# Kernel optimization log

Measured on AMD Instinct MI355X. Metric: run time of the kernel, lower is better.

The kernel has to match this reference:

```python
import jax, jax.numpy as jnp
import numpy as np

MEAN = jnp.array([0.0, 0.0, 0.0, 0.0, 0.0], dtype=jnp.float32)
STD = jnp.array([0.1, 0.1, 0.2, 0.2, 1.0], dtype=jnp.float32)


def setup_inputs() -> dict:
    key = jax.random.key(0)
    k1, k2 = jax.random.split(key)
    B, N = 8, 250000
    boxes = jax.random.normal(k1, (B, N, 5), dtype=jnp.float32)
    deltas = jax.random.normal(k2, (B, N, 5), dtype=jnp.float32)
    return {"boxes": boxes, "deltas": deltas}


def reference(boxes, deltas):
    B, N = boxes.shape[0], boxes.shape[1]
    widths = boxes[:, :, 2] - boxes[:, :, 0]
    heights = boxes[:, :, 3] - boxes[:, :, 1]
    ctr_x = boxes[:, :, 0] + 0.5 * widths
    ctr_y = boxes[:, :, 1] + 0.5 * heights
    alpha = boxes[:, :, 4]

    d = deltas * STD + MEAN  # fused elementwise denorm
    dx, dy, dw, dh, dalpha = d[:, :, 0], d[:, :, 1], d[:, :, 2], d[:, :, 3], d[:, :, 4]

    pred_ctr_x = ctr_x + dx * widths
    pred_ctr_y = ctr_y + dy * heights
    pred_w = jnp.exp(dw) * widths
    pred_h = jnp.exp(dh) * heights
    pred_alpha = jnp.arctan(dalpha) + alpha

    x1 = pred_ctr_x - 0.5 * pred_w
    y1 = pred_ctr_y - 0.5 * pred_h
    x4 = pred_ctr_x + 0.5 * pred_w
    y4 = pred_ctr_y + 0.5 * pred_h
    x2 = x1
    y2 = y4
    x3 = x4
    y3 = y1

    ones = jnp.ones_like(y4)
    # Faithful to original: torch.cat along dim 0 then view(B,N,3,4)
    pred_boxes = jnp.concatenate(
        [x1, x2, x3, x4, y1, y2, y3, y4, ones, ones, ones, ones], axis=0
    ).reshape(B, N, 3, 4)

    z = jnp.zeros_like(pred_ctr_x)
    o = jnp.ones_like(pred_ctr_x)
    # 3x3 homogeneous matrices, built along last axis (matches torch dim=-1 cat)
    T = jnp.stack([o, z, pred_ctr_x, z, o, pred_ctr_y, z, z, o], axis=-1).reshape(B, N, 3, 3)
    Tinv = jnp.stack([o, z, -pred_ctr_x, z, o, -pred_ctr_y, z, z, o], axis=-1).reshape(B, N, 3, 3)
    ca, sa = jnp.cos(pred_alpha), jnp.sin(pred_alpha)
    R = jnp.stack([ca, -sa, z, sa, ca, z, z, z, o], axis=-1).reshape(B, N, 3, 3)

    # [B,N,3,3] @ [B,N,3,4] chain, keep xy rows, transpose corners-last -> xy-last
    bbox_rotated = jnp.matmul(T, jnp.matmul(R, jnp.matmul(Tinv, pred_boxes)))[:, :, :2]
    return jnp.swapaxes(bbox_rotated, 2, 3)  # [B, N, 4, 2]
```

## Files before the change

kernel.cpp:

```cpp
#include <hip/hip_runtime.h>


typedef float    f4v __attribute__((ext_vector_type(4)));
typedef _Float16 h4v __attribute__((ext_vector_type(4)));
typedef _Float16 h8v __attribute__((ext_vector_type(8)));

__global__ __launch_bounds__(256) void bbox_phase1(
    const float* __restrict__ boxes, const float* __restrict__ deltas,
    _Float16* __restrict__ V, _Float16* __restrict__ CTR, int N, int total)
{
    int t = blockIdx.x * blockDim.x + threadIdx.x;
    int i0 = t * 4;
    if (i0 >= total) return;
    int b = i0 / N;
    int c = i0 - b * N;

    bool fast = (i0 + 3 < total) && (c + 3 < N) && ((c & 3) == 0) && ((N & 3) == 0);
    if (fast) {
        const f4v* bp = (const f4v*)(boxes  + (size_t)i0 * 5);
        const f4v* dp = (const f4v*)(deltas + (size_t)i0 * 5);
        float bv[20], dv[20];
        *(f4v*)&bv[0]  = bp[0]; *(f4v*)&bv[4]  = bp[1]; *(f4v*)&bv[8]  = bp[2];
        *(f4v*)&bv[12] = bp[3]; *(f4v*)&bv[16] = bp[4];
        *(f4v*)&dv[0]  = dp[0]; *(f4v*)&dv[4]  = dp[1]; *(f4v*)&dv[8]  = dp[2];
        *(f4v*)&dv[12] = dp[3]; *(f4v*)&dv[16] = dp[4];

        float X1[4], X4[4], Y1[4], Y4[4], PX[4], PY[4], CA[4], SA[4];
#pragma unroll
        for (int j = 0; j < 4; ++j) {
            float b0 = bv[j*5+0], b1 = bv[j*5+1], b2 = bv[j*5+2],
                  b3 = bv[j*5+3], b4 = bv[j*5+4];
            float d0 = dv[j*5+0], d1 = dv[j*5+1], d2 = dv[j*5+2],
                  d3 = dv[j*5+3], d4 = dv[j*5+4];
            float w  = b2 - b0, h = b3 - b1;
            float pcx = b0 + 0.5f * w + (d0 * 0.1f) * w;
            float pcy = b1 + 0.5f * h + (d1 * 0.1f) * h;
            float pw  = __expf(d2 * 0.2f) * w;
            float ph  = __expf(d3 * 0.2f) * h;
            X1[j] = pcx - 0.5f * pw;  X4[j] = pcx + 0.5f * pw;
            Y1[j] = pcy - 0.5f * ph;  Y4[j] = pcy + 0.5f * ph;
            float pal = atanf(d4) + b4;
            PX[j] = pcx; PY[j] = pcy;
            SA[j] = __sinf(pal); CA[j] = __cosf(pal);
        }
        size_t rs = (size_t)N;
        *(h4v*)(V + (size_t)(0*8 + b) * rs + c) =
            (h4v){(_Float16)X1[0],(_Float16)X1[1],(_Float16)X1[2],(_Float16)X1[3]};
        *(h4v*)(V + (size_t)(1*8 + b) * rs + c) =
            (h4v){(_Float16)X4[0],(_Float16)X4[1],(_Float16)X4[2],(_Float16)X4[3]};
        *(h4v*)(V + (size_t)(2*8 + b) * rs + c) =
            (h4v){(_Float16)Y1[0],(_Float16)Y1[1],(_Float16)Y1[2],(_Float16)Y1[3]};
        *(h4v*)(V + (size_t)(3*8 + b) * rs + c) =
            (h4v){(_Float16)Y4[0],(_Float16)Y4[1],(_Float16)Y4[2],(_Float16)Y4[3]};
        h8v ctrA = {(_Float16)PX[0],(_Float16)PY[0],(_Float16)CA[0],(_Float16)SA[0],
                    (_Float16)PX[1],(_Float16)PY[1],(_Float16)CA[1],(_Float16)SA[1]};
        h8v ctrB = {(_Float16)PX[2],(_Float16)PY[2],(_Float16)CA[2],(_Float16)SA[2],
                    (_Float16)PX[3],(_Float16)PY[3],(_Float16)CA[3],(_Float16)SA[3]};
        *(h8v*)(CTR + (size_t)i0 * 4)     = ctrA;
        *(h8v*)(CTR + (size_t)i0 * 4 + 8) = ctrB;
    } else {
#pragma unroll 1
        for (int j = 0; j < 4; ++j) {
            int i = i0 + j;
            if (i >= total) break;
            int bb = i / N, cc = i - bb * N;
            const float* bx = boxes  + (size_t)i * 5;
            const float* dl = deltas + (size_t)i * 5;
            float b0=bx[0],b1=bx[1],b2=bx[2],b3=bx[3],b4=bx[4];
            float d0=dl[0],d1=dl[1],d2=dl[2],d3=dl[3],d4=dl[4];
            float w = b2-b0, h = b3-b1;
            float pcx = b0 + 0.5f*w + (d0*0.1f)*w;
            float pcy = b1 + 0.5f*h + (d1*0.1f)*h;
            float pw = __expf(d2*0.2f)*w, ph = __expf(d3*0.2f)*h;
            size_t rs = (size_t)N;
            V[(size_t)(0*8+bb)*rs + cc] = (_Float16)(pcx - 0.5f*pw);
            V[(size_t)(1*8+bb)*rs + cc] = (_Float16)(pcx + 0.5f*pw);
            V[(size_t)(2*8+bb)*rs + cc] = (_Float16)(pcy - 0.5f*ph);
            V[(size_t)(3*8+bb)*rs + cc] = (_Float16)(pcy + 0.5f*ph);
            float pal = atanf(d4) + b4;
            CTR[(size_t)i*4 + 0] = (_Float16)pcx;
            CTR[(size_t)i*4 + 1] = (_Float16)pcy;
            CTR[(size_t)i*4 + 2] = (_Float16)__cosf(pal);
            CTR[(size_t)i*4 + 3] = (_Float16)__sinf(pal);
        }
    }
}

__global__ __launch_bounds__(256) void bbox_phase2(
    const _Float16* __restrict__ V, const _Float16* __restrict__ CTR,
    float* __restrict__ out, int N, int total)
{
    int t = blockIdx.x * blockDim.x + threadIdx.x;
    int i0 = t * 2;
    if (i0 >= total) return;

    int f = i0 * 12;
    int r = f / N;
    int c = f - r * N;
    bool pair = (i0 + 1 < total);

    float P[24];
    bool fast = pair && (c + 23 < N) && ((c & 7) == 0);
    if (fast) {
        if (r < 64) {
            int k = r >> 3, bb = r & 7;
            int v = (k < 4) ? (k >> 1) : (2 + (k & 1));
            const h8v* wp = (const h8v*)(V + (size_t)(v*8 + bb) * N + c);
            h8v a = wp[0], d = wp[1], e = wp[2];
#pragma unroll
            for (int j = 0; j < 8; ++j) {
                P[j]      = (float)a[j];
                P[8 + j]  = (float)d[j];
                P[16 + j] = (float)e[j];
            }
        } else {
#pragma unroll
            for (int j = 0; j < 24; ++j) P[j] = 1.0f;
        }
    } else {
#pragma unroll 1
        for (int j = 0; j < 24; ++j) {
            if (!pair && j >= 12) { P[j] = 1.0f; continue; }
            int ff = f + j;
            int rt = ff / N;
            int ct = ff - rt * N;
            if (rt >= 64) { P[j] = 1.0f; }
            else {
                int k = rt >> 3, bb = rt & 7;
                int v = (k < 4) ? (k >> 1) : (2 + (k & 1));
                P[j] = (float)V[(size_t)(v*8 + bb) * N + ct];
            }
        }
    }

    float pcx[2], pcy[2], cav[2], sav[2];
    if (pair) {
        h8v cc = *(const h8v*)(CTR + (size_t)i0 * 4);
        pcx[0]=(float)cc[0]; pcy[0]=(float)cc[1]; cav[0]=(float)cc[2]; sav[0]=(float)cc[3];
        pcx[1]=(float)cc[4]; pcy[1]=(float)cc[5]; cav[1]=(float)cc[6]; sav[1]=(float)cc[7];
    } else {
        pcx[0]=(float)CTR[(size_t)i0*4+0]; pcy[0]=(float)CTR[(size_t)i0*4+1];
        cav[0]=(float)CTR[(size_t)i0*4+2]; sav[0]=(float)CTR[(size_t)i0*4+3];
        pcx[1]=0.f; pcy[1]=0.f; cav[1]=1.f; sav[1]=0.f;
    }

#pragma unroll
    for (int q = 0; q < 2; ++q) {
        if (q && !pair) break;
        float r0o[4], r1o[4];
#pragma unroll
        for (int j = 0; j < 4; ++j) {
            float p0 = P[q*12 + j], p1 = P[q*12 + 4 + j], p2 = P[q*12 + 8 + j];
            float u0 = p0 - pcx[q] * p2;
            float u1 = p1 - pcy[q] * p2;
            float v0 = cav[q] * u0 - sav[q] * u1;
            float v1 = sav[q] * u0 + cav[q] * u1;
            r0o[j] = v0 + pcx[q] * p2;
            r1o[j] = v1 + pcy[q] * p2;
        }
        f4v* op = (f4v*)(out + (size_t)(i0 + q) * 8);
        op[0] = (f4v){r0o[0], r1o[0], r0o[1], r1o[1]};
        op[1] = (f4v){r0o[2], r1o[2], r0o[3], r1o[3]};
    }
}

__global__ __launch_bounds__(256) void bbox_fused_fallback(
    const float* __restrict__ boxes, const float* __restrict__ deltas,
    float* __restrict__ out, int N, int total)
{
    int idx = blockIdx.x * blockDim.x + threadIdx.x;
    if (idx >= total) return;
    int bp = idx / N;
    int n  = idx - bp * N;
    const float* bx = boxes  + (size_t)idx * 5;
    const float* dl = deltas + (size_t)idx * 5;
    float b0=bx[0],b1=bx[1],b2=bx[2],b3=bx[3],b4=bx[4];
    float d0=dl[0],d1=dl[1],d4=dl[4];
    float w=b2-b0, h=b3-b1;
    float pcx = b0+0.5f*w+(d0*0.1f)*w;
    float pcy = b1+0.5f*h+(d1*0.1f)*h;
    float pal = atanf(d4)+b4;
    float sa = __sinf(pal), ca = __cosf(pal);
    int m0 = n*12, q = m0/N, c0 = m0-q*N, r0 = bp*12+q;
    float P[12];
#pragma unroll
    for (int t = 0; t < 12; ++t) {
        int c = c0+t, r = r0;
        if (c >= N) { c -= N; r += 1; }
        float v;
        if (r >= 64) v = 1.0f;
        else {
            int k = r>>3, b = r&7;
            size_t base = ((size_t)b*N + c)*5;
            int a = (k<4)?0:1;
            float lo = boxes[base+a], hi = boxes[base+a+2];
            float dc = deltas[base+a], dd = deltas[base+a+2];
            float ww = hi-lo;
            float pc = lo+0.5f*ww+(dc*0.1f)*ww;
            float pwv = __expf(dd*0.2f)*ww;
            float s = ((0xAC>>k)&1)?0.5f:-0.5f;
            v = pc + s*pwv;
        }
        P[t] = v;
    }
    float r0o[4], r1o[4];
#pragma unroll
    for (int j = 0; j < 4; ++j) {
        float p0=P[j], p1=P[4+j], p2=P[8+j];
        float u0=p0-pcx*p2, u1=p1-pcy*p2;
        float v0=ca*u0-sa*u1, v1=sa*u0+ca*u1;
        r0o[j]=v0+pcx*p2; r1o[j]=v1+pcy*p2;
    }
    float4* op = (float4*)(out + (size_t)idx*8);
    op[0] = make_float4(r0o[0],r1o[0],r0o[1],r1o[1]);
    op[1] = make_float4(r0o[2],r1o[2],r0o[3],r1o[3]);
}

extern "C" void kernel_launch(void* const* d_in, const int* in_sizes, int n_in,
                              void* d_out, int out_size, void* d_ws, size_t ws_size,
                              hipStream_t stream) {
    const float* boxes  = (const float*)d_in[0];
    const float* deltas = (const float*)d_in[1];
    float* out = (float*)d_out;

    int total = in_sizes[0] / 5;
    int N = total / 8;
    int threads = 256;

    size_t vBytes   = (size_t)32 * N * sizeof(_Float16);
    size_t ctrBytes = (size_t)total * 4 * sizeof(_Float16);
    vBytes = (vBytes + 15) & ~(size_t)15;

    if (ws_size >= vBytes + ctrBytes) {
        _Float16* V   = (_Float16*)d_ws;
        _Float16* CTR = (_Float16*)((char*)d_ws + vBytes);
        int t1 = (total + 3) / 4;
        int blocks1 = (t1 + threads - 1) / threads;
        int t2 = (total + 1) / 2;
        int blocks2 = (t2 + threads - 1) / threads;
        bbox_phase1<<<blocks1, threads, 0, stream>>>(boxes, deltas, V, CTR, N, total);
        bbox_phase2<<<blocks2, threads, 0, stream>>>(V, CTR, out, N, total);
    } else {
        int blocks = (total + threads - 1) / threads;
        bbox_fused_fallback<<<blocks, threads, 0, stream>>>(boxes, deltas, out, N, total);
    }
}
```

Baseline: 51.51 us.

## Fuse both phases into one cooperative kernel with a grid-wide sync

Merges the two-kernel pipeline into a single cooperative launch of 1024 persistent blocks. Each block grid-strides through phase 1, all blocks meet at a grid barrier, then they grid-stride through phase 2. This removes the second kernel launch and its gap, at the cost of the grid sync and reduced occupancy from the fixed block count. The phase-1 fast-path check is also relaxed by dropping the per-row alignment conditions, and the old two-kernel path is kept as a fallback if the cooperative launch fails.

```diff
diff --git a/kernel.cpp b/kernel.cpp
--- a/kernel.cpp
+++ b/kernel.cpp
@@ -1,21 +1,19 @@
 #include <hip/hip_runtime.h>
+#include <hip/hip_cooperative_groups.h>
+
+namespace cg = cooperative_groups;
 
 
 typedef float    f4v __attribute__((ext_vector_type(4)));
 typedef _Float16 h4v __attribute__((ext_vector_type(4)));
 typedef _Float16 h8v __attribute__((ext_vector_type(8)));
 
-__global__ __launch_bounds__(256) void bbox_phase1(
-    const float* __restrict__ boxes, const float* __restrict__ deltas,
-    _Float16* __restrict__ V, _Float16* __restrict__ CTR, int N, int total)
-{
-    int t = blockIdx.x * blockDim.x + threadIdx.x;
-    int i0 = t * 4;
-    if (i0 >= total) return;
-    int b = i0 / N;
-    int c = i0 - b * N;
-
-    bool fast = (i0 + 3 < total) && (c + 3 < N) && ((c & 3) == 0) && ((N & 3) == 0);
+__device__ __forceinline__ void phase1_quad(
+    const float* __restrict__ boxes, const float* __restrict__ deltas,
+    _Float16* __restrict__ V, _Float16* __restrict__ CTR, int N, int total,
+    int i0)
+{
+    bool fast = (i0 + 3 < total) && ((N & 3) == 0);
     if (fast) {
         const f4v* bp = (const f4v*)(boxes  + (size_t)i0 * 5);
         const f4v* dp = (const f4v*)(deltas + (size_t)i0 * 5);
@@ -43,6 +41,8 @@
             PX[j] = pcx; PY[j] = pcy;
             SA[j] = __sinf(pal); CA[j] = __cosf(pal);
         }
+        int b = i0 / N;
+        int c = i0 - b * N;
         size_t rs = (size_t)N;
         *(h4v*)(V + (size_t)(0*8 + b) * rs + c) =
             (h4v){(_Float16)X1[0],(_Float16)X1[1],(_Float16)X1[2],(_Float16)X1[3]};
@@ -86,14 +86,10 @@
     }
 }
 
-__global__ __launch_bounds__(256) void bbox_phase2(
+__device__ __forceinline__ void phase2_pair(
     const _Float16* __restrict__ V, const _Float16* __restrict__ CTR,
-    float* __restrict__ out, int N, int total)
-{
-    int t = blockIdx.x * blockDim.x + threadIdx.x;
-    int i0 = t * 2;
-    if (i0 >= total) return;
-
+    float* __restrict__ out, int N, int total, int i0)
+{
     int f = i0 * 12;
     int r = f / N;
     int c = f - r * N;
@@ -162,6 +158,45 @@
         op[0] = (f4v){r0o[0], r1o[0], r0o[1], r1o[1]};
         op[1] = (f4v){r0o[2], r1o[2], r0o[3], r1o[3]};
     }
+}
+
+__global__ __launch_bounds__(256) void bbox_coop(
+    const float* __restrict__ boxes, const float* __restrict__ deltas,
+    _Float16* __restrict__ V, _Float16* __restrict__ CTR,
+    float* __restrict__ out, int N, int total)
+{
+    int gsize = gridDim.x * blockDim.x;
+    int gtid  = blockIdx.x * blockDim.x + threadIdx.x;
+
+    int nquads = (total + 3) >> 2;
+    for (int q = gtid; q < nquads; q += gsize)
+        phase1_quad(boxes, deltas, V, CTR, N, total, q * 4);
+
+    cg::this_grid().sync();
+
+    int npairs = (total + 1) >> 1;
+    for (int p = gtid; p < npairs; p += gsize)
+        phase2_pair(V, CTR, out, N, total, p * 2);
+}
+
+__global__ __launch_bounds__(256) void bbox_phase1(
+    const float* __restrict__ boxes, const float* __restrict__ deltas,
+    _Float16* __restrict__ V, _Float16* __restrict__ CTR, int N, int total)
+{
+    int t = blockIdx.x * blockDim.x + threadIdx.x;
+    int i0 = t * 4;
+    if (i0 >= total) return;
+    phase1_quad(boxes, deltas, V, CTR, N, total, i0);
+}
+
+__global__ __launch_bounds__(256) void bbox_phase2(
+    const _Float16* __restrict__ V, const _Float16* __restrict__ CTR,
+    float* __restrict__ out, int N, int total)
+{
+    int t = blockIdx.x * blockDim.x + threadIdx.x;
+    int i0 = t * 2;
+    if (i0 >= total) return;
+    phase2_pair(V, CTR, out, N, total, i0);
 }
 
 __global__ __launch_bounds__(256) void bbox_fused_fallback(
@@ -234,6 +269,16 @@
     if (ws_size >= vBytes + ctrBytes) {
         _Float16* V   = (_Float16*)d_ws;
         _Float16* CTR = (_Float16*)((char*)d_ws + vBytes);
+
+        int nblk = 1024;
+        void* args[] = {(void*)&boxes, (void*)&deltas, (void*)&V, (void*)&CTR,
+                        (void*)&out, (void*)&N, (void*)&total};
+        hipError_t e = hipLaunchCooperativeKernel((const void*)bbox_coop,
+                                                  dim3(nblk), dim3(threads),
+                                                  args, 0, stream);
+        if (e == hipSuccess) return;
+        (void)hipGetLastError();
+
         int t1 = (total + 3) / 4;
         int blocks1 = (t1 + threads - 1) / threads;
         int t2 = (total + 1) / 2;
```

Result: slower. 199.9 us (+288.1%).

## Compute constant-ones output region directly in phase1, shrink phase2 grid

Applied to the files above, without the earlier changes.

Output elements whose pred_boxes input is the constant 'ones' rows (indices at or beyond iOnes) are now written straight from phase1 in fp32, without going through the fp16 CTR buffer and phase2. Phase2 is launched only over the first two thirds of elements. This removes the CTR write and read for that third of the work plus phase2 threads that loaded nothing useful. Phase1 now does the extra output stores, and its fast-path condition is loosened by dropping the per-batch alignment checks.

```diff
diff --git a/kernel.cpp b/kernel.cpp
--- a/kernel.cpp
+++ b/kernel.cpp
@@ -5,17 +5,30 @@
 typedef _Float16 h4v __attribute__((ext_vector_type(4)));
 typedef _Float16 h8v __attribute__((ext_vector_type(8)));
 
+__device__ __forceinline__ void ones_out(float pcx, float pcy, float ca, float sa,
+                                         float* __restrict__ op)
+{
+    float u0 = 1.0f - pcx;
+    float u1 = 1.0f - pcy;
+    float v0 = ca * u0 - sa * u1;
+    float v1 = sa * u0 + ca * u1;
+    float r0 = v0 + pcx;
+    float r1 = v1 + pcy;
+    f4v val = (f4v){r0, r1, r0, r1};
+    ((f4v*)op)[0] = val;
+    ((f4v*)op)[1] = val;
+}
+
 __global__ __launch_bounds__(256) void bbox_phase1(
     const float* __restrict__ boxes, const float* __restrict__ deltas,
-    _Float16* __restrict__ V, _Float16* __restrict__ CTR, int N, int total)
+    _Float16* __restrict__ V, _Float16* __restrict__ CTR,
+    float* __restrict__ out, int N, int total, int iOnes)
 {
     int t = blockIdx.x * blockDim.x + threadIdx.x;
     int i0 = t * 4;
     if (i0 >= total) return;
-    int b = i0 / N;
-    int c = i0 - b * N;
-
-    bool fast = (i0 + 3 < total) && (c + 3 < N) && ((c & 3) == 0) && ((N & 3) == 0);
+
+    bool fast = (i0 + 3 < total) && ((N & 3) == 0);
     if (fast) {
         const f4v* bp = (const f4v*)(boxes  + (size_t)i0 * 5);
         const f4v* dp = (const f4v*)(deltas + (size_t)i0 * 5);
@@ -43,6 +56,8 @@
             PX[j] = pcx; PY[j] = pcy;
             SA[j] = __sinf(pal); CA[j] = __cosf(pal);
         }
+        int b = i0 / N;
+        int c = i0 - b * N;
         size_t rs = (size_t)N;
         *(h4v*)(V + (size_t)(0*8 + b) * rs + c) =
             (h4v){(_Float16)X1[0],(_Float16)X1[1],(_Float16)X1[2],(_Float16)X1[3]};
@@ -52,12 +67,32 @@
             (h4v){(_Float16)Y1[0],(_Float16)Y1[1],(_Float16)Y1[2],(_Float16)Y1[3]};
         *(h4v*)(V + (size_t)(3*8 + b) * rs + c) =
             (h4v){(_Float16)Y4[0],(_Float16)Y4[1],(_Float16)Y4[2],(_Float16)Y4[3]};
-        h8v ctrA = {(_Float16)PX[0],(_Float16)PY[0],(_Float16)CA[0],(_Float16)SA[0],
-                    (_Float16)PX[1],(_Float16)PY[1],(_Float16)CA[1],(_Float16)SA[1]};
-        h8v ctrB = {(_Float16)PX[2],(_Float16)PY[2],(_Float16)CA[2],(_Float16)SA[2],
-                    (_Float16)PX[3],(_Float16)PY[3],(_Float16)CA[3],(_Float16)SA[3]};
-        *(h8v*)(CTR + (size_t)i0 * 4)     = ctrA;
-        *(h8v*)(CTR + (size_t)i0 * 4 + 8) = ctrB;
+
+        if (i0 + 3 < iOnes) {
+            h8v ctrA = {(_Float16)PX[0],(_Float16)PY[0],(_Float16)CA[0],(_Float16)SA[0],
+                        (_Float16)PX[1],(_Float16)PY[1],(_Float16)CA[1],(_Float16)SA[1]};
+            h8v ctrB = {(_Float16)PX[2],(_Float16)PY[2],(_Float16)CA[2],(_Float16)SA[2],
+                        (_Float16)PX[3],(_Float16)PY[3],(_Float16)CA[3],(_Float16)SA[3]};
+            *(h8v*)(CTR + (size_t)i0 * 4)     = ctrA;
+            *(h8v*)(CTR + (size_t)i0 * 4 + 8) = ctrB;
+        } else if (i0 >= iOnes) {
+#pragma unroll
+            for (int j = 0; j < 4; ++j)
+                ones_out(PX[j], PY[j], CA[j], SA[j], out + (size_t)(i0 + j) * 8);
+        } else {
+#pragma unroll 1
+            for (int j = 0; j < 4; ++j) {
+                int i = i0 + j;
+                if (i < iOnes) {
+                    CTR[(size_t)i*4 + 0] = (_Float16)PX[j];
+                    CTR[(size_t)i*4 + 1] = (_Float16)PY[j];
+                    CTR[(size_t)i*4 + 2] = (_Float16)CA[j];
+                    CTR[(size_t)i*4 + 3] = (_Float16)SA[j];
+                } else {
+                    ones_out(PX[j], PY[j], CA[j], SA[j], out + (size_t)i * 8);
+                }
+            }
+        }
     } else {
 #pragma unroll 1
         for (int j = 0; j < 4; ++j) {
@@ -78,26 +113,31 @@
             V[(size_t)(2*8+bb)*rs + cc] = (_Float16)(pcy - 0.5f*ph);
             V[(size_t)(3*8+bb)*rs + cc] = (_Float16)(pcy + 0.5f*ph);
             float pal = atanf(d4) + b4;
-            CTR[(size_t)i*4 + 0] = (_Float16)pcx;
-            CTR[(size_t)i*4 + 1] = (_Float16)pcy;
-            CTR[(size_t)i*4 + 2] = (_Float16)__cosf(pal);
-            CTR[(size_t)i*4 + 3] = (_Float16)__sinf(pal);
+            float ca = __cosf(pal), sa = __sinf(pal);
+            if (i < iOnes) {
+                CTR[(size_t)i*4 + 0] = (_Float16)pcx;
+                CTR[(size_t)i*4 + 1] = (_Float16)pcy;
+                CTR[(size_t)i*4 + 2] = (_Float16)ca;
+                CTR[(size_t)i*4 + 3] = (_Float16)sa;
+            } else {
+                ones_out(pcx, pcy, ca, sa, out + (size_t)i * 8);
+            }
         }
     }
 }
 
 __global__ __launch_bounds__(256) void bbox_phase2(
     const _Float16* __restrict__ V, const _Float16* __restrict__ CTR,
-    float* __restrict__ out, int N, int total)
+    float* __restrict__ out, int N, int limit)
 {
     int t = blockIdx.x * blockDim.x + threadIdx.x;
     int i0 = t * 2;
-    if (i0 >= total) return;
+    if (i0 >= limit) return;
 
     int f = i0 * 12;
     int r = f / N;
     int c = f - r * N;
-    bool pair = (i0 + 1 < total);
+    bool pair = (i0 + 1 < limit);
 
     float P[24];
     bool fast = pair && (c + 23 < N) && ((c & 7) == 0);
@@ -227,6 +267,9 @@
     int N = total / 8;
     int threads = 256;
 
+    int iOnes = (int)(((long)64 * N + 11) / 12);
+    if (iOnes > total) iOnes = total;
+
     size_t vBytes   = (size_t)32 * N * sizeof(_Float16);
     size_t ctrBytes = (size_t)total * 4 * sizeof(_Float16);
     vBytes = (vBytes + 15) & ~(size_t)15;
@@ -236,10 +279,11 @@
         _Float16* CTR = (_Float16*)((char*)d_ws + vBytes);
         int t1 = (total + 3) / 4;
         int blocks1 = (t1 + threads - 1) / threads;
-        int t2 = (total + 1) / 2;
+        int t2 = (iOnes + 1) / 2;
         int blocks2 = (t2 + threads - 1) / threads;
-        bbox_phase1<<<blocks1, threads, 0, stream>>>(boxes, deltas, V, CTR, N, total);
-        bbox_phase2<<<blocks2, threads, 0, stream>>>(V, CTR, out, N, total);
+        bbox_phase1<<<blocks1, threads, 0, stream>>>(boxes, deltas, V, CTR, out, N, total, iOnes);
+        if (blocks2 > 0)
+            bbox_phase2<<<blocks2, threads, 0, stream>>>(V, CTR, out, N, iOnes);
     } else {
         int blocks = (total + threads - 1) / threads;
         bbox_fused_fallback<<<blocks, threads, 0, stream>>>(boxes, deltas, out, N, total);
```

Measured after the change: 51.64 us. No clear change (+0.3%).
